# Kernel tuning notes

Hardware: AMD Instinct MI355X
Metric: run time of the kernel (lower is better)

Reference implementation:

```python
import jax, jax.numpy as jnp
import numpy as np

N_EMBD = 256


def setup_inputs() -> dict:
    key = jax.random.key(0)
    kx, kq, kk, kv = jax.random.split(key, 4)
    B, S, D = 4, 4096, N_EMBD
    scale = 1.0 / np.sqrt(D)
    x = jax.random.normal(kx, (B, S, D), dtype=jnp.float32)
    # nn.Linear(D, D, bias=False) weights; torch applies x @ W.T
    Wq = jax.random.normal(kq, (D, D), dtype=jnp.float32) * scale
    Wk = jax.random.normal(kk, (D, D), dtype=jnp.float32) * scale
    Wv = jax.random.normal(kv, (D, D), dtype=jnp.float32) * scale
    return {"x": x, "Wq": Wq, "Wk": Wk, "Wv": Wv}


def reference(x, Wq, Wk, Wv):
    B, S, D = x.shape
    q = jnp.einsum('bsd,ed->bse', x, Wq)
    k = jnp.einsum('bsd,ed->bse', x, Wk)
    v = jnp.einsum('bsd,ed->bse', x, Wv)
    scale = 1.0 / jnp.sqrt(jnp.asarray(D, dtype=x.dtype))
    scores = jnp.einsum('bqd,bkd->bqk', q, k) * scale  # [B,S,S]
    causal = jnp.tril(jnp.ones((S, S), dtype=bool))
    masked = jnp.where(causal[None, :, :], scores, jnp.asarray(-jnp.inf, dtype=scores.dtype))
    weights = jax.nn.softmax(masked, axis=-1)
    out = jnp.einsum('bqk,bkd->bqd', weights, v)
    return out
```

## Files before the change

### kernel.cpp

```cpp
#include <hip/hip_runtime.h>
#include <hip/hip_bf16.h>


#define SEQ 4096
#define DIM 256
#define NBATCH 4
#define KVBLK 64
#define KVT_BYTES 65536

#define QB_OFF   0
#define KV_OFF   (8u*1024*1024)
#define O1_OFF   (24u*1024*1024)
#define O2_OFF   (32u*1024*1024)
#define O3_OFF   (40u*1024*1024)
#define ML_OFF   (48u*1024*1024)

#define QSCALE 0.09016844f
#define DEFER_THR 11.5415603f

typedef __attribute__((ext_vector_type(8))) short bf16x8;
typedef __attribute__((ext_vector_type(4))) float f32x4;
typedef __attribute__((ext_vector_type(4))) unsigned short us4;

static __device__ inline unsigned short f2bf(float f) {
  unsigned int u = __float_as_uint(f);
  u += 0x7FFFu + ((u >> 16) & 1u);
  return (unsigned short)(u >> 16);
}
static __device__ inline float bf2f(unsigned short u) {
  return __uint_as_float(((unsigned int)u) << 16);
}

__global__ __launch_bounds__(256) void qkv_gemm(
    const float* __restrict__ x, const float* __restrict__ Wq,
    const float* __restrict__ Wk, const float* __restrict__ Wv,
    char* __restrict__ qbf, char* __restrict__ kv)
{
  __shared__ unsigned short A_lds[128][40];
  __shared__ unsigned short B_lds[3][64][40];

  const int tid = threadIdx.x;
  const int lane = tid & 63;
  const int w = tid >> 6;
  const int lo = lane & 15, hi = lane >> 4;
  const int mb = blockIdx.x * 128;
  const int nb = blockIdx.y * 64;
  const float* Ws[3] = { Wq, Wk, Wv };

  f32x4 acc[3][2][4];
#pragma unroll
  for (int z = 0; z < 3; z++)
#pragma unroll
    for (int mi = 0; mi < 2; mi++)
#pragma unroll
      for (int ni = 0; ni < 4; ni++) acc[z][mi][ni] = (f32x4){0.f, 0.f, 0.f, 0.f};

  for (int ks = 0; ks < 8; ++ks) {
    const int k0 = ks * 32;
    __syncthreads();
#pragma unroll
    for (int i = 0; i < 4; ++i) {
      int f = tid + i * 256;
      int row = f >> 3, c4 = (f & 7) * 4;
      float4 v = *(const float4*)(x + (size_t)(mb + row) * DIM + k0 + c4);
      us4 bv = { f2bf(v.x), f2bf(v.y), f2bf(v.z), f2bf(v.w) };
      *(us4*)&A_lds[row][c4] = bv;
    }
#pragma unroll
    for (int z = 0; z < 3; z++)
#pragma unroll
      for (int i = 0; i < 2; ++i) {
        int f = tid + i * 256;
        int row = f >> 3, c4 = (f & 7) * 4;
        float4 v = *(const float4*)(Ws[z] + (size_t)(nb + row) * DIM + k0 + c4);
        us4 bv = { f2bf(v.x), f2bf(v.y), f2bf(v.z), f2bf(v.w) };
        *(us4*)&B_lds[z][row][c4] = bv;
      }
    __syncthreads();
    bf16x8 a[2];
#pragma unroll
    for (int mi = 0; mi < 2; mi++) a[mi] = *(const bf16x8*)&A_lds[w * 32 + mi * 16 + lo][hi * 8];
#pragma unroll
    for (int z = 0; z < 3; z++) {
      bf16x8 bfr[4];
#pragma unroll
      for (int ni = 0; ni < 4; ni++) bfr[ni] = *(const bf16x8*)&B_lds[z][ni * 16 + lo][hi * 8];
#pragma unroll
      for (int mi = 0; mi < 2; mi++)
#pragma unroll
        for (int ni = 0; ni < 4; ni++)
          acc[z][mi][ni] = __builtin_amdgcn_mfma_f32_16x16x32_bf16(a[mi], bfr[ni], acc[z][mi][ni], 0, 0, 0);
    }
  }

#pragma unroll
  for (int mi = 0; mi < 2; mi++) {
    int r0 = mb + w * 32 + mi * 16 + hi * 4;
#pragma unroll
    for (int ni = 0; ni < 4; ni++) {
      int d = nb + ni * 16 + lo;
      int kkq = d >> 5, hiq = (d >> 3) & 3, eq = d & 7;
#pragma unroll
      for (int j = 0; j < 4; j++) {
        int srow = r0 + j;
        int s16 = srow >> 4, loq = srow & 15;
        size_t byte = ((size_t)(s16 * 8 + kkq) << 10) + ((hiq * 16 + loq) << 4) + eq * 2;
        *(unsigned short*)(qbf + byte) = f2bf(acc[0][mi][ni][j] * QSCALE);
      }
    }
  }
#pragma unroll
  for (int mi = 0; mi < 2; mi++) {
    int r0 = mb + w * 32 + mi * 16 + hi * 4;
#pragma unroll
    for (int ni = 0; ni < 4; ni++) {
      int d = nb + ni * 16 + lo;
      int kkk = d >> 5, hik = (d >> 3) & 3, ek = d & 7;
#pragma unroll
      for (int j = 0; j < 4; j++) {
        int srow = r0 + j;
        int bb = srow >> 12, sl = srow & 4095;
        int t = sl >> 6, r = sl & 63;
        int nf = r >> 4, lok = r & 15;
        size_t byte = ((size_t)(bb * 64 + t)) * KVT_BYTES +
                      ((size_t)(nf * 8 + kkk) << 10) + ((hik * 16 + lok) << 4) + ek * 2;
        *(unsigned short*)(kv + byte) = f2bf(acc[1][mi][ni][j]);
      }
    }
  }
#pragma unroll
  for (int mi = 0; mi < 2; mi++) {
    int s0 = mb + w * 32 + mi * 16 + hi * 4;
    int bb = s0 >> 12;
    int t = (s0 >> 6) & 63;
    int s_t = s0 & 63;
    int ksI = s_t >> 5;
    int hf = (s_t >> 3) & 3;
    int e0 = s_t & 7;
#pragma unroll
    for (int ni = 0; ni < 4; ni++) {
      int d = nb + ni * 16 + lo;
      int n = d >> 4;
      us4 pv = { f2bf(acc[2][mi][ni][0]), f2bf(acc[2][mi][ni][1]),
                 f2bf(acc[2][mi][ni][2]), f2bf(acc[2][mi][ni][3]) };
      size_t byte = ((size_t)(bb * 64 + t)) * KVT_BYTES + 32768 +
                    ((size_t)(ksI * 16 + n) << 10) + ((hf * 16 + lo) << 4) + e0 * 2;
      *(us4*)(kv + byte) = pv;
    }
  }
}

__global__ __launch_bounds__(512, 1) void attn_fa(
    const char* __restrict__ qbf, const char* __restrict__ kv,
    float* __restrict__ out, unsigned short* __restrict__ o1,
    unsigned short* __restrict__ o2, unsigned short* __restrict__ o3,
    float* __restrict__ ml)
{
  __shared__ char KV_lds[2][KVT_BYTES];
  __shared__ unsigned short P_lds[8][16][88];

  const int tid = threadIdx.x;
  const int lane = tid & 63;
  const int w = tid >> 6;
  const int lo = lane & 15, hi = lane >> 4;
  const int id = blockIdx.x;
  const int x = id & 7;
  const int b = x >> 1;
  const int v = id >> 3;
  const int p = v & 15;
  const int cbase = ((v >> 4) << 1) | (x & 1);

  const char* kv_base = kv + (size_t)b * 64 * KVT_BYTES;

  auto stageKV = [&](int t, int buf) {
    const char* src = kv_base + (size_t)t * KVT_BYTES + tid * 16;
    char* dst = &KV_lds[buf][0] + tid * 16;
#pragma unroll
    for (int i = 0; i < 8; ++i) {
      __builtin_amdgcn_global_load_lds(
          (const __attribute__((address_space(1))) void*)(src + i * 8192),
          (__attribute__((address_space(3))) void*)(dst + i * 8192),
          16, 0, 0);
    }
  };

  for (int task = 0; task < 2; ++task) {
    const int u = task ? (15 - p) + 16 : p;
    const int cc = task ? (3 - cbase) : cbase;
    const int nt = 2 * u + 2;
    const int t0 = (nt * cc) >> 2;
    const int t1 = (nt * (cc + 1)) >> 2;
    const int qrow0 = u * 128 + w * 16;
    const int rbase = b * SEQ + qrow0;
    float* mlc = ml + (size_t)cc * 16384 * 2;

    if (t0 >= t1) {
      if (lane < 16) {
        mlc[(size_t)(rbase + lane) * 2 + 0] = -3e38f;
        mlc[(size_t)(rbase + lane) * 2 + 1] = 0.f;
      }
      if (cc == 0) {
#pragma unroll
        for (int j = 0; j < 16; j++)
#pragma unroll
          for (int n = 0; n < 4; n++)
            out[(size_t)(rbase + j) * DIM + n * 64 + lane] = 0.f;
      }
      continue;
    }

    bf16x8 qf[8];
    {
      const char* qp = qbf + ((size_t)(b * 256 + u * 8 + w) << 13) + lane * 16;
#pragma unroll
      for (int kk = 0; kk < 8; kk++)
        qf[kk] = *(const bf16x8*)(qp + kk * 1024);
    }

    stageKV(t0, 0);
    if (t0 + 1 < t1) stageKV(t0 + 1, 1);

    float m_run = -3e38f, l_run = 0.f;
    f32x4 o_acc[16];
#pragma unroll
    for (int n = 0; n < 16; n++) o_acc[n] = (f32x4){0.f, 0.f, 0.f, 0.f};

    for (int t = t0; t < t1; ++t) {
      const int cur = (t - t0) & 1;

      if (t + 1 < t1) {
        asm volatile("s_waitcnt vmcnt(8)" ::: "memory");
      } else {
        asm volatile("s_waitcnt vmcnt(0)" ::: "memory");
      }
      __builtin_amdgcn_sched_barrier(0);
      __builtin_amdgcn_s_barrier();

      const char* kt = &KV_lds[cur][0] + lane * 16;

      f32x4 sfT[4];
      __builtin_amdgcn_s_setprio(1);
#pragma unroll
      for (int nf = 0; nf < 4; nf++) {
        bf16x8 kf[8];
#pragma unroll
        for (int kk = 0; kk < 8; kk++)
          kf[kk] = *(const bf16x8*)(kt + ((nf * 8 + kk) << 10));
        f32x4 a = (f32x4){0.f, 0.f, 0.f, 0.f};
#pragma unroll
        for (int kk = 0; kk < 8; kk++)
          a = __builtin_amdgcn_mfma_f32_16x16x32_bf16(kf[kk], qf[kk], a, 0, 0, 0);
        sfT[nf] = a;
      }
      __builtin_amdgcn_s_setprio(0);

      const char* vt = &KV_lds[cur][32768] + lane * 16;
      bf16x8 va[16];
#pragma unroll
      for (int i = 0; i < 16; i++)
        va[i] = *(const bf16x8*)(vt + (i << 10));

      if ((t * KVBLK + KVBLK - 1) > qrow0) {
        int qg = qrow0 + lo;
#pragma unroll
        for (int nf = 0; nf < 4; nf++) {
#pragma unroll
          for (int j = 0; j < 4; j++) {
            int kg = t * KVBLK + nf * 16 + hi * 4 + j;
            if (kg > qg) sfT[nf][j] = -__builtin_inff();
          }
        }
      }

      float vnew = sfT[0][0];
#pragma unroll
      for (int nf = 0; nf < 4; nf++)
#pragma unroll
        for (int j = 0; j < 4; j++) vnew = fmaxf(vnew, sfT[nf][j]);
      vnew = fmaxf(vnew, __shfl_xor(vnew, 16));
      vnew = fmaxf(vnew, __shfl_xor(vnew, 32));

      if (__any(vnew > m_run + DEFER_THR)) {
        float mn = fmaxf(m_run, vnew);
        float alpha = exp2f(m_run - mn);
        m_run = mn;
        l_run *= alpha;
#pragma unroll
        for (int j = 0; j < 4; j++) {
          float aj = __shfl(alpha, (lane & 48) + ((lane >> 4) & 3) * 4 + j);
#pragma unroll
          for (int n = 0; n < 16; n++) o_acc[n][j] *= aj;
        }
      }
      {
        float sum = 0.f;
#pragma unroll
        for (int nf = 0; nf < 4; nf++)
#pragma unroll
          for (int j = 0; j < 4; j++) {
            sfT[nf][j] = exp2f(sfT[nf][j] - m_run);
            sum += sfT[nf][j];
          }
        l_run += sum;
      }

#pragma unroll
      for (int nf = 0; nf < 4; nf++) {
#pragma unroll
        for (int h2 = 0; h2 < 2; h2++) {
          unsigned int pk;
          asm("v_cvt_pk_bf16_f32 %0, %1, %2"
              : "=v"(pk) : "v"(sfT[nf][h2 * 2]), "v"(sfT[nf][h2 * 2 + 1]));
          *(unsigned int*)&P_lds[w][lo][nf * 16 + hi * 4 + h2 * 2] = pk;
        }
      }
      bf16x8 pa0 = *(const bf16x8*)&P_lds[w][lo][hi * 8];
      bf16x8 pa1 = *(const bf16x8*)&P_lds[w][lo][32 + hi * 8];

      __builtin_amdgcn_s_setprio(1);
#pragma unroll
      for (int g = 0; g < 4; g++) {
        bf16x8 vb[4];
#pragma unroll
        for (int k = 0; k < 4; k++)
          vb[k] = *(const bf16x8*)(vt + ((16 + g * 4 + k) << 10));
#pragma unroll
        for (int k = 0; k < 4; k++) {
          int n = g * 4 + k;
          o_acc[n] = __builtin_amdgcn_mfma_f32_16x16x32_bf16(pa0, va[n], o_acc[n], 0, 0, 0);
          o_acc[n] = __builtin_amdgcn_mfma_f32_16x16x32_bf16(pa1, vb[k], o_acc[n], 0, 0, 0);
        }
      }
      __builtin_amdgcn_s_setprio(0);

      __builtin_amdgcn_sched_barrier(0);
      __builtin_amdgcn_s_barrier();
      if (t + 2 < t1) stageKV(t + 2, cur);
    }

    l_run += __shfl_xor(l_run, 16);
    l_run += __shfl_xor(l_run, 32);
    float inv = (l_run > 0.f) ? 1.f / l_run : 0.f;

    unsigned short* opc = (cc == 1) ? o1 : (cc == 2) ? o2 : o3;
#pragma unroll
    for (int j = 0; j < 4; j++) {
      float invj = __shfl(inv, (lane & 48) + ((lane >> 4) & 3) * 4 + j);
      int r = rbase + hi * 4 + j;
      if (cc == 0) {
        float* orow = out + (size_t)r * DIM;
#pragma unroll
        for (int n = 0; n < 16; n++)
          orow[n * 16 + lo] = o_acc[n][j] * invj;
      } else {
        unsigned short* orow = opc + (size_t)r * DIM;
#pragma unroll
        for (int n = 0; n < 16; n++)
          orow[n * 16 + lo] = f2bf(o_acc[n][j] * invj);
      }
    }
    if (hi == 0) {
      mlc[(size_t)(rbase + lo) * 2 + 0] = m_run;
      mlc[(size_t)(rbase + lo) * 2 + 1] = l_run;
    }
  }
}

__global__ __launch_bounds__(256) void merge4(
    const float* __restrict__ ml,
    const unsigned short* __restrict__ o1, const unsigned short* __restrict__ o2,
    const unsigned short* __restrict__ o3, float* __restrict__ out)
{
  int r = blockIdx.x * 4 + (threadIdx.x >> 6);
  int c4 = (threadIdx.x & 63) * 4;
  float m0 = ml[(size_t)r*2],           l0 = ml[(size_t)r*2+1];
  float m1 = ml[(size_t)(16384+r)*2],   l1 = ml[(size_t)(16384+r)*2+1];
  float m2 = ml[(size_t)(32768+r)*2],   l2 = ml[(size_t)(32768+r)*2+1];
  float m3 = ml[(size_t)(49152+r)*2],   l3 = ml[(size_t)(49152+r)*2+1];
  float M = fmaxf(fmaxf(m0, m1), fmaxf(m2, m3));
  float w0 = l0 * exp2f(m0 - M);
  float w1 = l1 * exp2f(m1 - M);
  float w2 = l2 * exp2f(m2 - M);
  float w3 = l3 * exp2f(m3 - M);
  float inv = 1.f / (w0 + w1 + w2 + w3);
  float4 o0 = *(const float4*)(out + (size_t)r * DIM + c4);
  us4 a  = *(const us4*)(o1 + (size_t)r * DIM + c4);
  us4 bq = *(const us4*)(o2 + (size_t)r * DIM + c4);
  us4 cq = *(const us4*)(o3 + (size_t)r * DIM + c4);
  float4 res;
  res.x = (w0*o0.x + w1*bf2f(a.x) + w2*bf2f(bq.x) + w3*bf2f(cq.x)) * inv;
  res.y = (w0*o0.y + w1*bf2f(a.y) + w2*bf2f(bq.y) + w3*bf2f(cq.y)) * inv;
  res.z = (w0*o0.z + w1*bf2f(a.z) + w2*bf2f(bq.z) + w3*bf2f(cq.z)) * inv;
  res.w = (w0*o0.w + w1*bf2f(a.w) + w2*bf2f(bq.w) + w3*bf2f(cq.w)) * inv;
  *(float4*)(out + (size_t)r * DIM + c4) = res;
}

extern "C" void kernel_launch(void* const* d_in, const int* in_sizes, int n_in,
                              void* d_out, int out_size, void* d_ws, size_t ws_size,
                              hipStream_t stream) {
  const float* x  = (const float*)d_in[0];
  const float* Wq = (const float*)d_in[1];
  const float* Wk = (const float*)d_in[2];
  const float* Wv = (const float*)d_in[3];
  char* ws = (char*)d_ws;
  char* qbf = ws + QB_OFF;
  char* kv  = ws + KV_OFF;
  unsigned short* o1 = (unsigned short*)(ws + O1_OFF);
  unsigned short* o2 = (unsigned short*)(ws + O2_OFF);
  unsigned short* o3 = (unsigned short*)(ws + O3_OFF);
  float* ml = (float*)(ws + ML_OFF);
  float* out = (float*)d_out;

  qkv_gemm<<<dim3(128, 4), 256, 0, stream>>>(x, Wq, Wk, Wv, qbf, kv);
  attn_fa<<<dim3(256), 512, 0, stream>>>(qbf, kv, out, o1, o2, o3, ml);
  merge4<<<dim3(4096), 256, 0, stream>>>(ml, o1, o2, o3, out);
}
```

Before: 86.40 us.

## Split KV tile softmax into two halves to overlap PV MFMA with exp

Each 64-key tile is now processed as two 32-key halves, each with its own max, rescale, exp and P write. The first half's PV MFMAs are issued before the second half's softmax runs, so matrix work can overlap with the vector exp and shuffle work. This adds a second online-softmax rescale check per tile and keeps two score fragments live. The P_lds row padding is also reduced from 88 to 72 elements, which changes the LDS bank mapping.

```diff
diff --git a/kernel.cpp b/kernel.cpp
--- a/kernel.cpp
+++ b/kernel.cpp
@@ -157,7 +157,7 @@
     float* __restrict__ ml)
 {
   __shared__ char KV_lds[2][KVT_BYTES];
-  __shared__ unsigned short P_lds[8][16][88];
+  __shared__ unsigned short P_lds[8][16][72];
 
   const int tid = threadIdx.x;
   const int lane = tid & 63;
@@ -237,11 +237,14 @@
       __builtin_amdgcn_s_barrier();
 
       const char* kt = &KV_lds[cur][0] + lane * 16;
-
-      f32x4 sfT[4];
+      const char* vt = &KV_lds[cur][32768] + lane * 16;
+      const bool needmask = (t * KVBLK + KVBLK - 1) > qrow0;
+      const int qg = qrow0 + lo;
+
+      f32x4 sfT0[2];
       __builtin_amdgcn_s_setprio(1);
 #pragma unroll
-      for (int nf = 0; nf < 4; nf++) {
+      for (int nf = 0; nf < 2; nf++) {
         bf16x8 kf[8];
 #pragma unroll
         for (int kk = 0; kk < 8; kk++)
@@ -250,71 +253,132 @@
 #pragma unroll
         for (int kk = 0; kk < 8; kk++)
           a = __builtin_amdgcn_mfma_f32_16x16x32_bf16(kf[kk], qf[kk], a, 0, 0, 0);
-        sfT[nf] = a;
+        sfT0[nf] = a;
+      }
+      f32x4 sfT1[2];
+#pragma unroll
+      for (int nf = 2; nf < 4; nf++) {
+        bf16x8 kf[8];
+#pragma unroll
+        for (int kk = 0; kk < 8; kk++)
+          kf[kk] = *(const bf16x8*)(kt + ((nf * 8 + kk) << 10));
+        f32x4 a = (f32x4){0.f, 0.f, 0.f, 0.f};
+#pragma unroll
+        for (int kk = 0; kk < 8; kk++)
+          a = __builtin_amdgcn_mfma_f32_16x16x32_bf16(kf[kk], qf[kk], a, 0, 0, 0);
+        sfT1[nf - 2] = a;
       }
       __builtin_amdgcn_s_setprio(0);
 
-      const char* vt = &KV_lds[cur][32768] + lane * 16;
       bf16x8 va[16];
 #pragma unroll
       for (int i = 0; i < 16; i++)
         va[i] = *(const bf16x8*)(vt + (i << 10));
 
-      if ((t * KVBLK + KVBLK - 1) > qrow0) {
-        int qg = qrow0 + lo;
-#pragma unroll
-        for (int nf = 0; nf < 4; nf++) {
+      if (needmask) {
+#pragma unroll
+        for (int nf = 0; nf < 2; nf++)
 #pragma unroll
           for (int j = 0; j < 4; j++) {
             int kg = t * KVBLK + nf * 16 + hi * 4 + j;
-            if (kg > qg) sfT[nf][j] = -__builtin_inff();
+            if (kg > qg) sfT0[nf][j] = -__builtin_inff();
+          }
+      }
+      {
+        float vnew = sfT0[0][0];
+#pragma unroll
+        for (int nf = 0; nf < 2; nf++)
+#pragma unroll
+          for (int j = 0; j < 4; j++) vnew = fmaxf(vnew, sfT0[nf][j]);
+        vnew = fmaxf(vnew, __shfl_xor(vnew, 16));
+        vnew = fmaxf(vnew, __shfl_xor(vnew, 32));
+        if (__any(vnew > m_run + DEFER_THR)) {
+          float mn = fmaxf(m_run, vnew);
+          float alpha = exp2f(m_run - mn);
+          m_run = mn;
+          l_run *= alpha;
+#pragma unroll
+          for (int j = 0; j < 4; j++) {
+            float aj = __shfl(alpha, (lane & 48) + ((lane >> 4) & 3) * 4 + j);
+#pragma unroll
+            for (int n = 0; n < 16; n++) o_acc[n][j] *= aj;
           }
         }
-      }
-
-      float vnew = sfT[0][0];
-#pragma unroll
-      for (int nf = 0; nf < 4; nf++)
-#pragma unroll
-        for (int j = 0; j < 4; j++) vnew = fmaxf(vnew, sfT[nf][j]);
-      vnew = fmaxf(vnew, __shfl_xor(vnew, 16));
-      vnew = fmaxf(vnew, __shfl_xor(vnew, 32));
-
-      if (__any(vnew > m_run + DEFER_THR)) {
-        float mn = fmaxf(m_run, vnew);
-        float alpha = exp2f(m_run - mn);
-        m_run = mn;
-        l_run *= alpha;
-#pragma unroll
-        for (int j = 0; j < 4; j++) {
-          float aj = __shfl(alpha, (lane & 48) + ((lane >> 4) & 3) * 4 + j);
-#pragma unroll
-          for (int n = 0; n < 16; n++) o_acc[n][j] *= aj;
-        }
-      }
-      {
         float sum = 0.f;
 #pragma unroll
-        for (int nf = 0; nf < 4; nf++)
-#pragma unroll
-          for (int j = 0; j < 4; j++) {
-            sfT[nf][j] = exp2f(sfT[nf][j] - m_run);
-            sum += sfT[nf][j];
+        for (int nf = 0; nf < 2; nf++)
+#pragma unroll
+          for (int j = 0; j < 4; j++) {
+            sfT0[nf][j] = exp2f(sfT0[nf][j] - m_run);
+            sum += sfT0[nf][j];
           }
         l_run += sum;
       }
-
-#pragma unroll
-      for (int nf = 0; nf < 4; nf++) {
+#pragma unroll
+      for (int nf = 0; nf < 2; nf++)
 #pragma unroll
         for (int h2 = 0; h2 < 2; h2++) {
           unsigned int pk;
           asm("v_cvt_pk_bf16_f32 %0, %1, %2"
-              : "=v"(pk) : "v"(sfT[nf][h2 * 2]), "v"(sfT[nf][h2 * 2 + 1]));
+              : "=v"(pk) : "v"(sfT0[nf][h2 * 2]), "v"(sfT0[nf][h2 * 2 + 1]));
           *(unsigned int*)&P_lds[w][lo][nf * 16 + hi * 4 + h2 * 2] = pk;
         }
-      }
       bf16x8 pa0 = *(const bf16x8*)&P_lds[w][lo][hi * 8];
+
+      __builtin_amdgcn_s_setprio(1);
+#pragma unroll
+      for (int n = 0; n < 16; n++)
+        o_acc[n] = __builtin_amdgcn_mfma_f32_16x16x32_bf16(pa0, va[n], o_acc[n], 0, 0, 0);
+      __builtin_amdgcn_s_setprio(0);
+
+      if (needmask) {
+#pragma unroll
+        for (int nf = 0; nf < 2; nf++)
+#pragma unroll
+          for (int j = 0; j < 4; j++) {
+            int kg = t * KVBLK + (nf + 2) * 16 + hi * 4 + j;
+            if (kg > qg) sfT1[nf][j] = -__builtin_inff();
+          }
+      }
+      {
+        float vnew = sfT1[0][0];
+#pragma unroll
+        for (int nf = 0; nf < 2; nf++)
+#pragma unroll
+          for (int j = 0; j < 4; j++) vnew = fmaxf(vnew, sfT1[nf][j]);
+        vnew = fmaxf(vnew, __shfl_xor(vnew, 16));
+        vnew = fmaxf(vnew, __shfl_xor(vnew, 32));
+        if (__any(vnew > m_run + DEFER_THR)) {
+          float mn = fmaxf(m_run, vnew);
+          float alpha = exp2f(m_run - mn);
+          m_run = mn;
+          l_run *= alpha;
+#pragma unroll
+          for (int j = 0; j < 4; j++) {
+            float aj = __shfl(alpha, (lane & 48) + ((lane >> 4) & 3) * 4 + j);
+#pragma unroll
+            for (int n = 0; n < 16; n++) o_acc[n][j] *= aj;
+          }
+        }
+        float sum = 0.f;
+#pragma unroll
+        for (int nf = 0; nf < 2; nf++)
+#pragma unroll
+          for (int j = 0; j < 4; j++) {
+            sfT1[nf][j] = exp2f(sfT1[nf][j] - m_run);
+            sum += sfT1[nf][j];
+          }
+        l_run += sum;
+      }
+#pragma unroll
+      for (int nf = 0; nf < 2; nf++)
+#pragma unroll
+        for (int h2 = 0; h2 < 2; h2++) {
+          unsigned int pk;
+          asm("v_cvt_pk_bf16_f32 %0, %1, %2"
+              : "=v"(pk) : "v"(sfT1[nf][h2 * 2]), "v"(sfT1[nf][h2 * 2 + 1]));
+          *(unsigned int*)&P_lds[w][lo][32 + nf * 16 + hi * 4 + h2 * 2] = pk;
+        }
       bf16x8 pa1 = *(const bf16x8*)&P_lds[w][lo][32 + hi * 8];
 
       __builtin_amdgcn_s_setprio(1);
@@ -327,7 +391,6 @@
 #pragma unroll
         for (int k = 0; k < 4; k++) {
           int n = g * 4 + k;
-          o_acc[n] = __builtin_amdgcn_mfma_f32_16x16x32_bf16(pa0, va[n], o_acc[n], 0, 0, 0);
           o_acc[n] = __builtin_amdgcn_mfma_f32_16x16x32_bf16(pa1, vb[k], o_acc[n], 0, 0, 0);
         }
       }
```

Measured after the change: 91.42 us. +5.8%, slower.
